# Kernel tuning notes

Measured on AMD Instinct MI355X. Metric: run time of the kernel, lower is better.

## Reference

```python
import jax, jax.numpy as jnp
import numpy as np
import math

BS, S, E, H, DK = 32, 512, 512, 8, 64


def setup_inputs() -> dict:
    key = jax.random.key(0)
    ks = jax.random.split(key, 10)
    q = jax.random.normal(ks[0], (BS, S, E), jnp.float32)
    k = jax.random.normal(ks[1], (BS, S, E), jnp.float32)
    v = jax.random.normal(ks[2], (BS, S, E), jnp.float32)
    # strictly-causal mask: allowed where col < row (np.triu(k=0)==0)
    mask = jnp.tril(jnp.ones((S, S), bool), -1)[None, None]
    sc = 1.0 / math.sqrt(E)  # xavier-ish scale for square linears
    Wq = jax.random.normal(ks[3], (E, E), jnp.float32) * sc
    Wk = jax.random.normal(ks[4], (E, E), jnp.float32) * sc
    Wv = jax.random.normal(ks[5], (E, E), jnp.float32) * sc
    Wo = jax.random.normal(ks[6], (E, E), jnp.float32) * sc
    bq = jnp.zeros((E,), jnp.float32)
    bk = jnp.zeros((E,), jnp.float32)
    bv = jnp.zeros((E,), jnp.float32)
    bo = jnp.zeros((E,), jnp.float32)
    gammas = jax.random.normal(ks[7], (H, 1, 1), jnp.float32) * 0.5
    return {"q": q, "k": k, "v": v, "mask": mask, "zero_pad": 1,
            "Wq": Wq, "bq": bq, "Wk": Wk, "bk": bk, "Wv": Wv, "bv": bv,
            "Wo": Wo, "bo": bo, "gammas": gammas}


def reference(q, k, v, mask, zero_pad, Wq, bq, Wk, bk, Wv, bv, Wo, bo, gammas):
    bs = q.shape[0]
    # projections (torch Linear: x @ W.T + b), split heads -> [b,h,s,d]
    def heads(x, W, b):
        return (x @ W.T + b).reshape(bs, S, H, DK).transpose(0, 2, 1, 3)
    qh, kh, vh = heads(q, Wq, bq), heads(k, Wk, bk), heads(v, Wv, bv)

    scores = jnp.einsum('bhqd,bhkd->bhqk', qh, kh) / math.sqrt(DK)

    # --- distance-decay term (no-grad in original) ---
    neg = jnp.float32(-1e32)
    scores_ = jnp.where(mask, scores, neg)
    scores_ = jax.nn.softmax(scores_, axis=-1) * mask.astype(scores.dtype)
    distcum = jnp.cumsum(scores_, axis=-1)
    disttotal = jnp.sum(scores_, axis=-1, keepdims=True)
    idx = jnp.arange(S)
    position_effect = jnp.abs(idx[None, :] - idx[:, None]).astype(scores.dtype)[None, None]
    dist_scores = jnp.sqrt(jnp.clip((disttotal - distcum) * position_effect, 0.0))
    dist_scores = jax.lax.stop_gradient(dist_scores)

    gamma = -jax.nn.softplus(gammas)[None]  # [1,h,1,1]
    total_effect = jnp.clip(jnp.exp(dist_scores * gamma), 1e-5, 1e5)

    scores = scores * total_effect
    scores = jnp.where(mask, scores, neg)
    scores = jax.nn.softmax(scores, axis=-1)
    if zero_pad:
        scores = scores.at[:, :, 0, :].set(0.0)

    out = jnp.einsum('bhqk,bhkd->bhqd', scores, vh)
    concat = out.transpose(0, 2, 1, 3).reshape(bs, S, E)
    return concat @ Wo.T + bo
```

## Files before the change

kernel.cpp:

```cpp
#include <hip/hip_runtime.h>
#include <hip/hip_bf16.h>
#include <hip/hip_fp16.h>
#include <stdint.h>

#define BSZ 32
#define SEQ 512
#define EMB 512
#define NH  8
#define DKD 64
#define LOG2E 1.4426950408889634f

typedef float f32x4 __attribute__((ext_vector_type(4)));
typedef short s16x8 __attribute__((ext_vector_type(8)));

#if __has_builtin(__builtin_amdgcn_exp2f)
#define EXP2(x) __builtin_amdgcn_exp2f(x)
#else
#define EXP2(x) exp2f(x)
#endif
#define RCP(x) __builtin_amdgcn_rcpf(x)

__device__ inline unsigned short f2bf(float f) {
  union { float f; unsigned u; } v; v.f = f;
  unsigned r = v.u + 0x7fffu + ((v.u >> 16) & 1u);
  return (unsigned short)(r >> 16);
}

__device__ inline ushort4 pack4bf(float4 v) {
  union { __hip_bfloat162 h2[2]; ushort4 u4; } cv;
  cv.h2[0] = __float22bfloat162_rn(make_float2(v.x, v.y));
  cv.h2[1] = __float22bfloat162_rn(make_float2(v.z, v.w));
  return cv.u4;
}

__device__ inline void stage16(const void* g, void* l) {
#if defined(__has_builtin) && __has_builtin(__builtin_amdgcn_global_load_lds)
  __builtin_amdgcn_global_load_lds(
      (const __attribute__((address_space(1))) void*)g,
      (__attribute__((address_space(3))) void*)l, 16, 0, 0);
#else
  *reinterpret_cast<uint4*>(l) = *reinterpret_cast<const uint4*>(g);
#endif
}

template<int CTRL>
__device__ inline float dpp_shr_f(float x) {
  return __builtin_bit_cast(float,
    __builtin_amdgcn_update_dpp(0, __builtin_bit_cast(int, x), CTRL, 0xf, 0xf, true));
}
__device__ inline float rlane(float v, int l) {
  return __builtin_bit_cast(float, __builtin_amdgcn_readlane(__builtin_bit_cast(int, v), l));
}

__global__ __launch_bounds__(256)
void wcvt(const float* __restrict__ w0, const float* __restrict__ w1,
          const float* __restrict__ w2, const float* __restrict__ w3,
          unsigned short* __restrict__ o0, unsigned short* __restrict__ o1,
          unsigned short* __restrict__ o2, unsigned short* __restrict__ o3)
{
  const float* src = (blockIdx.y == 0) ? w0 : (blockIdx.y == 1) ? w1
                   : (blockIdx.y == 2) ? w2 : w3;
  unsigned short* dst = (blockIdx.y == 0) ? o0 : (blockIdx.y == 1) ? o1
                      : (blockIdx.y == 2) ? o2 : o3;
  const int i = (blockIdx.x * 256 + threadIdx.x) * 8;
  float4 a = *reinterpret_cast<const float4*>(src + i);
  float4 b = *reinterpret_cast<const float4*>(src + i + 4);
  union { ushort4 p[2]; s16x8 v; } cc;
  cc.p[0] = pack4bf(a); cc.p[1] = pack4bf(b);
  *reinterpret_cast<s16x8*>(dst + i) = cc.v;
}

__global__ __launch_bounds__(256)
void proj_gemm(const float* __restrict__ q, const float* __restrict__ k,
               const float* __restrict__ v,
               const unsigned short* __restrict__ Wq,
               const unsigned short* __restrict__ Wk,
               const unsigned short* __restrict__ Wv,
               const float* __restrict__ bq, const float* __restrict__ bk,
               const float* __restrict__ bv,
               unsigned short* __restrict__ Qh, unsigned short* __restrict__ Kh,
               unsigned short* __restrict__ Vt, float qscale)
{
  __shared__ __align__(16) char smem[2 * 24576];
  const int tid  = threadIdx.x;
  const int lane = tid & 63;
  const int w    = tid >> 6;
  const int lin  = blockIdx.x;
  const int x    = lin & 7;
  const int j    = lin >> 3;
  const int P    = x * 48 + (j >> 2);
  const int proj = P >> 7;
  const int m0   = (P & 127) * 128;
  const int n0   = (j & 3) * 128;
  const float* A = (proj == 0) ? q : (proj == 1) ? k : v;
  const unsigned short* Bw = (proj == 0) ? Wq : (proj == 1) ? Wk : Wv;
  const float* bias = (proj == 0) ? bq : (proj == 1) ? bk : bv;
  const float oscale = (proj == 0) ? qscale : 1.0f;
  const int K = EMB;

  const int wr   = (w >> 1) * 64;
  const int wc   = (w & 1) * 64;
  const int base = w * 1024 + lane * 16;

  auto stage = [&](int buf, int k0) {
    char* sA = smem + buf * 24576;
    char* sB = sA + 16384;
    #pragma unroll
    for (int c = 0; c < 4; ++c) {
      const int flat = c * 4096 + base;
      const int row  = flat >> 7;
      const int gl   = ((flat >> 4) & 7) ^ (row & 7);
      stage16(&A[(size_t)(m0 + row) * K + k0 + gl * 4], sA + flat);
    }
    #pragma unroll
    for (int c = 0; c < 2; ++c) {
      const int flat = c * 4096 + base;
      const int r    = flat >> 7;
      const int gl   = ((flat >> 4) & 7) ^ (r & 7);
      const int nn   = r + ((gl >> 2) << 6);
      stage16(&Bw[(size_t)(n0 + nn) * K + k0 + (gl & 3) * 8], sB + flat);
    }
  };

  f32x4 acc[4][4] = {};
  auto compute = [&](int buf) {
    char* sA = smem + buf * 24576;
    char* sB = sA + 16384;
    s16x8 af[4], bf[4];
    #pragma unroll
    for (int i = 0; i < 4; ++i) {
      const int row = wr + i * 16 + (lane & 15);
      const int g1  = (lane >> 4) << 1;
      float4 v1 = *reinterpret_cast<const float4*>(sA + row * 128 + ((g1 ^ (row & 7)) << 4));
      float4 v2 = *reinterpret_cast<const float4*>(sA + row * 128 + (((g1 + 1) ^ (row & 7)) << 4));
      union { ushort4 p[2]; s16x8 vv; } cc;
      cc.p[0] = pack4bf(v1); cc.p[1] = pack4bf(v2);
      af[i] = cc.vv;
    }
    #pragma unroll
    for (int jj = 0; jj < 4; ++jj) {
      const int n  = wc + jj * 16 + (lane & 15);
      const int r  = n & 63;
      const int gl = ((n >> 6) << 2) + (lane >> 4);
      bf[jj] = *reinterpret_cast<const s16x8*>(sB + r * 128 + ((gl ^ (r & 7)) << 4));
    }
    #pragma unroll
    for (int i = 0; i < 4; ++i)
      #pragma unroll
      for (int jj = 0; jj < 4; ++jj)
        acc[i][jj] = __builtin_amdgcn_mfma_f32_16x16x32_bf16(af[i], bf[jj], acc[i][jj], 0, 0, 0);
  };

  stage(0, 0);
  int cur = 0;
  for (int t = 0; t < 15; ++t) {
    stage(cur ^ 1, (t + 1) * 32);
    asm volatile("s_waitcnt vmcnt(6)" ::: "memory");
    __builtin_amdgcn_s_barrier();
    __builtin_amdgcn_sched_barrier(0);
    compute(cur);
    asm volatile("s_waitcnt lgkmcnt(0)" ::: "memory");
    __builtin_amdgcn_s_barrier();
    cur ^= 1;
  }
  asm volatile("s_waitcnt vmcnt(0)" ::: "memory");
  __builtin_amdgcn_s_barrier();
  __builtin_amdgcn_sched_barrier(0);
  compute(cur);

  #pragma unroll
  for (int i = 0; i < 4; ++i)
    #pragma unroll
    for (int jj = 0; jj < 4; ++jj)
      #pragma unroll
      for (int r = 0; r < 4; ++r) {
        const int gm = m0 + wr + i * 16 + (lane >> 4) * 4 + r;
        const int gn = n0 + wc + jj * 16 + (lane & 15);
        const float vv = (acc[i][jj][r] + bias[gn]) * oscale;
        const int b = gm >> 9, s = gm & 511, h = gn >> 6, d = gn & 63;
        if (proj == 2)
          Vt[((size_t)(b * NH + h) * DKD + d) * SEQ + s] = f2bf(vv);
        else if (proj == 1)
          Kh[((size_t)(b * NH + h) * SEQ + s) * DKD + d] = f2bf(vv);
        else
          Qh[((size_t)(b * NH + h) * SEQ + s) * DKD + d] = f2bf(vv);
      }
}

__global__ __launch_bounds__(256)
void out_gemm(const unsigned short* __restrict__ At,
              const unsigned short* __restrict__ Wo,
              const float* __restrict__ bo, float* __restrict__ C)
{
  __shared__ __align__(16) char smem[2 * 16384];
  const int tid  = threadIdx.x;
  const int lane = tid & 63;
  const int w    = tid >> 6;
  const int lin  = blockIdx.x;
  const int x    = lin & 7;
  const int j    = lin >> 3;
  const int P    = x * 16 + (j >> 2);
  const int m0   = P * 128;
  const int n0   = (j & 3) * 128;
  const int K = EMB, N = EMB;

  const int wr   = (w >> 1) * 64;
  const int wc   = (w & 1) * 64;
  const int base = w * 1024 + lane * 16;

  auto stage = [&](int buf, int k0) {
    char* sA = smem + buf * 16384;
    char* sB = sA + 8192;
    #pragma unroll
    for (int c = 0; c < 2; ++c) {
      const int flat = c * 4096 + base;
      const int r    = flat >> 7;
      const int gl   = ((flat >> 4) & 7) ^ (r & 7);
      const int row  = r + ((gl >> 2) << 6);
      stage16(&At[(size_t)(m0 + row) * K + k0 + (gl & 3) * 8], sA + flat);
    }
    #pragma unroll
    for (int c = 0; c < 2; ++c) {
      const int flat = c * 4096 + base;
      const int r    = flat >> 7;
      const int gl   = ((flat >> 4) & 7) ^ (r & 7);
      const int nn   = r + ((gl >> 2) << 6);
      stage16(&Wo[(size_t)(n0 + nn) * K + k0 + (gl & 3) * 8], sB + flat);
    }
  };

  f32x4 acc[4][4] = {};
  auto compute = [&](int buf) {
    char* sA = smem + buf * 16384;
    char* sB = sA + 8192;
    s16x8 af[4], bf[4];
    #pragma unroll
    for (int i = 0; i < 4; ++i) {
      const int row = wr + i * 16 + (lane & 15);
      const int r   = row & 63;
      const int gl  = ((row >> 6) << 2) + (lane >> 4);
      af[i] = *reinterpret_cast<const s16x8*>(sA + r * 128 + ((gl ^ (r & 7)) << 4));
    }
    #pragma unroll
    for (int jj = 0; jj < 4; ++jj) {
      const int n  = wc + jj * 16 + (lane & 15);
      const int r  = n & 63;
      const int gl = ((n >> 6) << 2) + (lane >> 4);
      bf[jj] = *reinterpret_cast<const s16x8*>(sB + r * 128 + ((gl ^ (r & 7)) << 4));
    }
    #pragma unroll
    for (int i = 0; i < 4; ++i)
      #pragma unroll
      for (int jj = 0; jj < 4; ++jj)
        acc[i][jj] = __builtin_amdgcn_mfma_f32_16x16x32_bf16(af[i], bf[jj], acc[i][jj], 0, 0, 0);
  };

  stage(0, 0);
  int cur = 0;
  for (int t = 0; t < 15; ++t) {
    stage(cur ^ 1, (t + 1) * 32);
    asm volatile("s_waitcnt vmcnt(4)" ::: "memory");
    __builtin_amdgcn_s_barrier();
    __builtin_amdgcn_sched_barrier(0);
    compute(cur);
    asm volatile("s_waitcnt lgkmcnt(0)" ::: "memory");
    __builtin_amdgcn_s_barrier();
    cur ^= 1;
  }
  asm volatile("s_waitcnt vmcnt(0)" ::: "memory");
  __builtin_amdgcn_s_barrier();
  __builtin_amdgcn_sched_barrier(0);
  compute(cur);

  #pragma unroll
  for (int i = 0; i < 4; ++i)
    #pragma unroll
    for (int jj = 0; jj < 4; ++jj)
      #pragma unroll
      for (int r = 0; r < 4; ++r) {
        const int gm = m0 + wr + i * 16 + (lane >> 4) * 4 + r;
        const int gn = n0 + wc + jj * 16 + (lane & 15);
        C[(size_t)gm * N + gn] = acc[i][jj][r] + bo[gn];
      }
}

template<int R>
__device__ inline void phase2_rows(unsigned short* s_lds, int w, int lane,
                                   int q0, int zp, float g2)
{
  constexpr int L  = 64 / R;
  constexpr int IT = 4 / R;
  const int seg = lane / L;
  const int li  = lane & (L - 1);
  const int jb  = li * 8;
  const float NEGINF = -__builtin_inff();
  #pragma unroll
  for (int it = 0; it < IT; ++it) {
    const int r  = w * 4 + it * R + seg;
    const int qg = q0 + r;
    const int gs = li ^ (r & 7);
    unsigned short* rowp = &s_lds[r * 512 + gs * 8];
    float pn2[8];
    if (qg == 0) {
      const float u = zp ? 0.0f : (1.0f / 512.0f);
      #pragma unroll
      for (int i = 0; i < 8; ++i) pn2[i] = u;
    } else {
      float sL[8];
      {
        s16x8 raw = *reinterpret_cast<const s16x8*>(rowp);
        union { s16x8 v; __half2 h[4]; } u; u.v = raw;
        #pragma unroll
        for (int i = 0; i < 4; ++i) {
          float2 f = __half22float2(u.h[i]);
          sL[2 * i] = f.x; sL[2 * i + 1] = f.y;
        }
      }
      #pragma unroll
      for (int i = 0; i < 8; ++i) sL[i] = (jb + i < qg) ? sL[i] : NEGINF;
      float p[8], c[8];
      float run = 0.f;
      #pragma unroll
      for (int i = 0; i < 8; ++i) { p[i] = EXP2(sL[i]); run += p[i]; c[i] = run; }
      float t = run;
      t += dpp_shr_f<0x111>(t);
      t += dpp_shr_f<0x112>(t);
      t += dpp_shr_f<0x114>(t);
      t += dpp_shr_f<0x118>(t);
      float tot;
      if constexpr (R == 1) {
        const float r0 = rlane(t, 15), r1 = rlane(t, 31), r2 = rlane(t, 47);
        const float a1 = r0, a2 = r0 + r1, a3 = a2 + r2;
        tot = a3 + rlane(t, 63);
        t += (lane >= 48) ? a3 : (lane >= 32) ? a2 : (lane >= 16) ? a1 : 0.f;
      } else if constexpr (R == 2) {
        const float r0 = rlane(t, 15), r2 = rlane(t, 47);
        t += (lane & 16) ? ((lane < 32) ? r0 : r2) : 0.f;
        tot = __shfl(t, lane | 31, 64);
      } else {
        tot = __shfl(t, lane | 15, 64);
      }
      const float pre  = tot - (t - run);
      const float g2r  = g2 * __builtin_amdgcn_sqrtf(RCP(tot));
      const float fb   = (float)(qg - jb);
      float p2[8]; float run2 = 0.f;
      #pragma unroll
      for (int i = 0; i < 8; ++i) {
        const float rem = pre - c[i];
        const float arg = fmaxf(rem * (fb - (float)i), 0.f);
        float te = EXP2(__builtin_amdgcn_sqrtf(arg) * g2r);
        te = fmaxf(te, 1e-5f);
        p2[i] = EXP2(sL[i] * te);
        run2 += p2[i];
      }
      float y = run2;
      y += dpp_shr_f<0x111>(y);
      y += dpp_shr_f<0x112>(y);
      y += dpp_shr_f<0x114>(y);
      y += dpp_shr_f<0x118>(y);
      float s2;
      if constexpr (R == 1) {
        s2 = rlane(y, 15) + rlane(y, 31) + rlane(y, 47) + rlane(y, 63);
      } else if constexpr (R == 2) {
        y += (lane & 16) ? ((lane < 32) ? rlane(y, 15) : rlane(y, 47)) : 0.f;
        s2 = __shfl(y, lane | 31, 64);
      } else {
        s2 = __shfl(y, lane | 15, 64);
      }
      const float inv2 = RCP(s2);
      #pragma unroll
      for (int i = 0; i < 8; ++i) pn2[i] = p2[i] * inv2;
    }
    union { __hip_bfloat162 h2[4]; uint4 u; } pk;
    pk.h2[0] = __float22bfloat162_rn(make_float2(pn2[0], pn2[1]));
    pk.h2[1] = __float22bfloat162_rn(make_float2(pn2[2], pn2[3]));
    pk.h2[2] = __float22bfloat162_rn(make_float2(pn2[4], pn2[5]));
    pk.h2[3] = __float22bfloat162_rn(make_float2(pn2[6], pn2[7]));
    *reinterpret_cast<uint4*>(rowp) = pk.u;
  }
}

__global__ __launch_bounds__(256)
void attn_kernel(const unsigned short* __restrict__ Qh,
                 const unsigned short* __restrict__ Kh,
                 const unsigned short* __restrict__ Vt,
                 unsigned short* __restrict__ Aout,
                 const float* __restrict__ gammas,
                 const int* __restrict__ zero_pad)
{
  __shared__ __align__(16) unsigned short s_lds[16 * 512];
  const int tid = threadIdx.x, lane = tid & 63, w = tid >> 6;
  const int lin = blockIdx.x;
  const int x   = lin & 7;
  const int u   = lin >> 3;
  const int qb  = u >> 5;
  const int h   = u & 7;
  const int b   = x * 4 + ((u >> 3) & 3);
  const int q0  = qb * 16;
  const size_t bh = (size_t)b * NH + h;
  const unsigned short* Qp = Qh + bh * SEQ * DKD;
  const unsigned short* Kp = Kh + bh * SEQ * DKD;
  const unsigned short* Vp = Vt + bh * DKD * SEQ;
  const int zp = zero_pad[0];
  const float g2 = -log1pf(__expf(gammas[h])) * LOG2E;

  s16x8 aq[2];
  #pragma unroll
  for (int kt = 0; kt < 2; ++kt)
    aq[kt] = *reinterpret_cast<const s16x8*>(&Qp[(q0 + (lane & 15)) * DKD + kt * 32 + (lane >> 4) * 8]);
  {
    const int frag = (lane >> 4) * 8;
    auto loadK = [&](int t, s16x8* kb) {
      const int n = t * 16 + (lane & 15);
      kb[0] = *reinterpret_cast<const s16x8*>(&Kp[n * DKD + frag]);
      kb[1] = *reinterpret_cast<const s16x8*>(&Kp[n * DKD + 32 + frag]);
    };
    auto tilecomp = [&](int t, const s16x8* kb) {
      f32x4 acc = {};
      acc = __builtin_amdgcn_mfma_f32_16x16x32_bf16(aq[0], kb[0], acc, 0, 0, 0);
      acc = __builtin_amdgcn_mfma_f32_16x16x32_bf16(aq[1], kb[1], acc, 0, 0, 0);
      const int n = t * 16 + (lane & 15);
      #pragma unroll
      for (int r = 0; r < 4; ++r) {
        const int row = (lane >> 4) * 4 + r;
        const int idx = row * 512 + ((((n >> 3) ^ (row & 7)) << 3) + (n & 7));
        s_lds[idx] = __half_as_ushort(__float2half(acc[r]));
      }
    };
    int t = w;
    if (t <= qb) {
      s16x8 cur[2], nxt[2];
      loadK(t, cur);
      while (true) {
        const int tn = t + 4;
        if (tn <= qb) {
          loadK(tn, nxt);
          tilecomp(t, cur);
          cur[0] = nxt[0]; cur[1] = nxt[1];
          t = tn;
        } else {
          tilecomp(t, cur);
          break;
        }
      }
    }
  }
  __syncthreads();

  if (zp == 0 && qb == 0) {
    phase2_rows<1>(s_lds, w, lane, q0, zp, g2);
  } else if (qb < 8) {
    phase2_rows<4>(s_lds, w, lane, q0, zp, g2);
  } else if (qb < 16) {
    phase2_rows<2>(s_lds, w, lane, q0, zp, g2);
  } else {
    phase2_rows<1>(s_lds, w, lane, q0, zp, g2);
  }
  __syncthreads();

  f32x4 oacc = {};
  const int row  = lane & 15;
  const int koff = lane >> 4;
  const int rsw  = row & 7;
  const unsigned short* vbase = &Vp[(w * 16 + row) * SEQ + koff * 8];
  const int ks_end = (qb == 0 && zp == 0) ? 16 : (qb >> 1) + 1;
  int ks0 = 0;
  for (; ks0 + 4 <= ks_end; ks0 += 4) {
    s16x8 vb[4], pa[4];
    #pragma unroll
    for (int uu = 0; uu < 4; ++uu) {
      const int ks = ks0 + uu;
      vb[uu] = *reinterpret_cast<const s16x8*>(&vbase[ks * 32]);
      pa[uu] = *reinterpret_cast<const s16x8*>(&s_lds[row * 512 + ((ks * 4 + koff) ^ rsw) * 8]);
    }
    #pragma unroll
    for (int uu = 0; uu < 4; ++uu)
      oacc = __builtin_amdgcn_mfma_f32_16x16x32_bf16(pa[uu], vb[uu], oacc, 0, 0, 0);
  }
  for (; ks0 < ks_end; ++ks0) {
    s16x8 vb = *reinterpret_cast<const s16x8*>(&vbase[ks0 * 32]);
    s16x8 pa = *reinterpret_cast<const s16x8*>(&s_lds[row * 512 + ((ks0 * 4 + koff) ^ rsw) * 8]);
    oacc = __builtin_amdgcn_mfma_f32_16x16x32_bf16(pa, vb, oacc, 0, 0, 0);
  }
  #pragma unroll
  for (int r = 0; r < 4; ++r) {
    const int orow = (lane >> 4) * 4 + r;
    const int ocol = w * 16 + (lane & 15);
    Aout[((size_t)b * SEQ + (q0 + orow)) * EMB + h * DKD + ocol] = f2bf(oacc[r]);
  }
}

extern "C" void kernel_launch(void* const* d_in, const int* in_sizes, int n_in,
                              void* d_out, int out_size, void* d_ws, size_t ws_size,
                              hipStream_t stream)
{
  const float* q  = (const float*)d_in[0];
  const float* k  = (const float*)d_in[1];
  const float* v  = (const float*)d_in[2];
  const int*   zp = (const int*)d_in[4];
  const float* Wq = (const float*)d_in[5];
  const float* bq = (const float*)d_in[6];
  const float* Wk = (const float*)d_in[7];
  const float* bk = (const float*)d_in[8];
  const float* Wv = (const float*)d_in[9];
  const float* bv = (const float*)d_in[10];
  const float* Wo = (const float*)d_in[11];
  const float* bo = (const float*)d_in[12];
  const float* gm = (const float*)d_in[13];

  char* ws = (char*)d_ws;
  const size_t HB = (size_t)BSZ * NH * SEQ * DKD * sizeof(unsigned short);
  const size_t WB = (size_t)EMB * EMB * sizeof(unsigned short);
  unsigned short* Qh  = (unsigned short*)(ws);
  unsigned short* Kh  = (unsigned short*)(ws + HB);
  unsigned short* Vt  = (unsigned short*)(ws + 2 * HB);
  unsigned short* At  = (unsigned short*)(ws + 3 * HB);
  unsigned short* Wqb = (unsigned short*)(ws + 4 * HB);
  unsigned short* Wkb = (unsigned short*)(ws + 4 * HB + WB);
  unsigned short* Wvb = (unsigned short*)(ws + 4 * HB + 2 * WB);
  unsigned short* Wob = (unsigned short*)(ws + 4 * HB + 3 * WB);

  wcvt<<<dim3(128, 4), 256, 0, stream>>>(Wq, Wk, Wv, Wo, Wqb, Wkb, Wvb, Wob);
  proj_gemm<<<1536, 256, 0, stream>>>(q, k, v, Wqb, Wkb, Wvb, bq, bk, bv,
                                      Qh, Kh, Vt, 0.125f * LOG2E);
  attn_kernel<<<8192, 256, 0, stream>>>(Qh, Kh, Vt, At, gm, zp);
  out_gemm<<<512, 256, 0, stream>>>(At, Wob, bo, (float*)d_out);
}
```

Measured before the change: 173.8 us.

## Single-buffer projection GEMM staging and remap block-to-tile assignment

Replaces the double-buffered LDS pipeline in the QKV projection GEMM with a single 24 KB buffer and a plain stage/sync/compute/sync loop. This halves shared memory per block, which may let more blocks share a CU, but it gives up overlapping global loads with MFMA compute. It also changes how block indices map to projection and row tiles, so each XCD-strided group now covers contiguous row tiles within one projection.

```diff
diff --git a/kernel.cpp b/kernel.cpp
--- a/kernel.cpp
+++ b/kernel.cpp
@@ -81,16 +81,19 @@
                unsigned short* __restrict__ Qh, unsigned short* __restrict__ Kh,
                unsigned short* __restrict__ Vt, float qscale)
 {
-  __shared__ __align__(16) char smem[2 * 24576];
+  __shared__ __align__(16) char smem[24576];
+  char* const sA = smem;
+  char* const sB = smem + 16384;
   const int tid  = threadIdx.x;
   const int lane = tid & 63;
   const int w    = tid >> 6;
   const int lin  = blockIdx.x;
   const int x    = lin & 7;
   const int j    = lin >> 3;
-  const int P    = x * 48 + (j >> 2);
-  const int proj = P >> 7;
-  const int m0   = (P & 127) * 128;
+  const int pp   = j >> 2;
+  const int proj = pp >> 4;
+  const int pl   = pp & 15;
+  const int m0   = (x * 16 + pl) * 128;
   const int n0   = (j & 3) * 128;
   const float* A = (proj == 0) ? q : (proj == 1) ? k : v;
   const unsigned short* Bw = (proj == 0) ? Wq : (proj == 1) ? Wk : Wv;
@@ -102,9 +105,7 @@
   const int wc   = (w & 1) * 64;
   const int base = w * 1024 + lane * 16;
 
-  auto stage = [&](int buf, int k0) {
-    char* sA = smem + buf * 24576;
-    char* sB = sA + 16384;
+  auto stage = [&](int k0) {
     #pragma unroll
     for (int c = 0; c < 4; ++c) {
       const int flat = c * 4096 + base;
@@ -123,9 +124,7 @@
   };
 
   f32x4 acc[4][4] = {};
-  auto compute = [&](int buf) {
-    char* sA = smem + buf * 24576;
-    char* sB = sA + 16384;
+  auto compute = [&]() {
     s16x8 af[4], bf[4];
     #pragma unroll
     for (int i = 0; i < 4; ++i) {
@@ -151,22 +150,12 @@
         acc[i][jj] = __builtin_amdgcn_mfma_f32_16x16x32_bf16(af[i], bf[jj], acc[i][jj], 0, 0, 0);
   };
 
-  stage(0, 0);
-  int cur = 0;
-  for (int t = 0; t < 15; ++t) {
-    stage(cur ^ 1, (t + 1) * 32);
-    asm volatile("s_waitcnt vmcnt(6)" ::: "memory");
-    __builtin_amdgcn_s_barrier();
-    __builtin_amdgcn_sched_barrier(0);
-    compute(cur);
-    asm volatile("s_waitcnt lgkmcnt(0)" ::: "memory");
-    __builtin_amdgcn_s_barrier();
-    cur ^= 1;
-  }
-  asm volatile("s_waitcnt vmcnt(0)" ::: "memory");
-  __builtin_amdgcn_s_barrier();
-  __builtin_amdgcn_sched_barrier(0);
-  compute(cur);
+  for (int t = 0; t < 16; ++t) {
+    stage(t * 32);
+    __syncthreads();
+    compute();
+    __syncthreads();
+  }
 
   #pragma unroll
   for (int i = 0; i < 4; ++i)
```

Measured after the change: 154.0 us. 1.13x faster.
